# Optimization experiments

Measured on AMD Instinct MI355X. Metric: run time of the kernel, lower is better.

Reference implementation:

```python
import jax, jax.numpy as jnp
import numpy as np

N = 4194304   # number of query coordinates
D = 8         # feature width of xs
V = 1048576   # number of active sparse entries (param table size)


def setup_inputs() -> dict:
    key = jax.random.key(0)
    k1, k2, k3 = jax.random.split(key, 3)
    xs = jax.random.normal(k1, (N, D), dtype=jnp.float32)
    idx = jax.random.randint(k2, (N,), 0, V, dtype=jnp.int64)
    params = jax.random.normal(k3, (V, 1), dtype=jnp.float32)  # one scalar param per sparse entry
    return {"xs": xs, "idx": idx, "params": params}


def reference(xs, idx, params):
    # Original torch loop: out[i] = params[idx[i]] * xs[i]; fused gather-multiply.
    return params[idx] * xs  # [N,1] broadcast against [N,D] -> [N,D]
```

## Files before the change

kernel.cpp:

```cpp
#include <hip/hip_runtime.h>


typedef float f32x4 __attribute__((ext_vector_type(4)));

__global__ __launch_bounds__(256) void spvar_kernel(
    const f32x4* __restrict__ xs4,
    const int*   __restrict__ idx,
    const float* __restrict__ params,
    f32x4*       __restrict__ out4,
    int nrows, int stride)
{
    const int t = blockIdx.x * blockDim.x + threadIdx.x;
    const int r0 = t;
    const int r1 = t + stride;
    const int r2 = t + 2 * stride;
    const int r3 = t + 3 * stride;

    if (r3 < nrows) {
        const int i0 = idx[r0];
        const int i1 = idx[r1];
        const int i2 = idx[r2];
        const int i3 = idx[r3];

        const float p0 = params[i0];
        const float p1 = params[i1];
        const float p2 = params[i2];
        const float p3 = params[i3];

        f32x4 a0 = xs4[2 * r0], b0 = xs4[2 * r0 + 1];
        f32x4 a1 = xs4[2 * r1], b1 = xs4[2 * r1 + 1];
        f32x4 a2 = xs4[2 * r2], b2 = xs4[2 * r2 + 1];
        f32x4 a3 = xs4[2 * r3], b3 = xs4[2 * r3 + 1];

        a0 *= p0; b0 *= p0;
        a1 *= p1; b1 *= p1;
        a2 *= p2; b2 *= p2;
        a3 *= p3; b3 *= p3;

        out4[2 * r0] = a0; out4[2 * r0 + 1] = b0;
        out4[2 * r1] = a1; out4[2 * r1 + 1] = b1;
        out4[2 * r2] = a2; out4[2 * r2 + 1] = b2;
        out4[2 * r3] = a3; out4[2 * r3 + 1] = b3;
    } else {
        #pragma unroll
        for (int u = 0; u < 4; ++u) {
            const int r = t + u * stride;
            if (r < nrows) {
                const float p = params[idx[r]];
                f32x4 a = xs4[2 * r];
                f32x4 b = xs4[2 * r + 1];
                a *= p; b *= p;
                out4[2 * r]     = a;
                out4[2 * r + 1] = b;
            }
        }
    }
}

extern "C" void kernel_launch(void* const* d_in, const int* in_sizes, int n_in,
                              void* d_out, int out_size, void* d_ws, size_t ws_size,
                              hipStream_t stream) {
    const float* xs     = (const float*)d_in[0];
    const int*   idx    = (const int*)d_in[1];
    const float* params = (const float*)d_in[2];

    const int nrows = out_size / 8;
    const int block = 256;
    const int rows_per_thread = 4;
    const int grid = (nrows + block * rows_per_thread - 1) / (block * rows_per_thread);
    const int stride = grid * block;

    spvar_kernel<<<grid, block, 0, stream>>>(
        (const f32x4*)xs, idx, params, (f32x4*)d_out, nrows, stride);
}
```

Baseline: 260.4 us.

## Bucket param gathers by table range and use nontemporal streaming loads/stores

Each thread now handles eight rows and loads all eight indices up front. It then gathers params in four passes, one per quarter of the table, with scheduling barriers between passes, so concurrent gathers hit a smaller slice of the table and stay cache-resident. The streaming xs loads, index loads and output stores become nontemporal so they do not evict the param table. This adds predicated extra passes and hardcodes the table size as VTAB, so it breaks if V changes. Launch bounds also now request higher occupancy.

```diff
diff --git a/kernel.cpp b/kernel.cpp
--- a/kernel.cpp
+++ b/kernel.cpp
@@ -3,7 +3,12 @@
 
 typedef float f32x4 __attribute__((ext_vector_type(4)));
 
-__global__ __launch_bounds__(256) void spvar_kernel(
+#define ROWS 8
+#define NB   4
+#define VTAB 1048576
+#define BSZ  (VTAB / NB)
+
+__global__ __launch_bounds__(256, 8) void spvar_kernel(
     const f32x4* __restrict__ xs4,
     const int*   __restrict__ idx,
     const float* __restrict__ params,
@@ -11,48 +16,37 @@
     int nrows, int stride)
 {
     const int t = blockIdx.x * blockDim.x + threadIdx.x;
-    const int r0 = t;
-    const int r1 = t + stride;
-    const int r2 = t + 2 * stride;
-    const int r3 = t + 3 * stride;
 
-    if (r3 < nrows) {
-        const int i0 = idx[r0];
-        const int i1 = idx[r1];
-        const int i2 = idx[r2];
-        const int i3 = idx[r3];
+    int   ix[ROWS];
+    float p[ROWS];
+    #pragma unroll
+    for (int u = 0; u < ROWS; ++u) {
+        const int r = t + u * stride;
+        ix[u] = (r < nrows) ? __builtin_nontemporal_load(idx + r) : -1;
+        p[u]  = 0.0f;
+    }
 
-        const float p0 = params[i0];
-        const float p1 = params[i1];
-        const float p2 = params[i2];
-        const float p3 = params[i3];
+    #pragma unroll
+    for (int b = 0; b < NB; ++b) {
+        const int lo = b * BSZ;
+        #pragma unroll
+        for (int u = 0; u < ROWS; ++u) {
+            if ((unsigned)(ix[u] - lo) < (unsigned)BSZ)
+                p[u] = params[ix[u]];
+        }
+        __builtin_amdgcn_sched_barrier(0);
+    }
 
-        f32x4 a0 = xs4[2 * r0], b0 = xs4[2 * r0 + 1];
-        f32x4 a1 = xs4[2 * r1], b1 = xs4[2 * r1 + 1];
-        f32x4 a2 = xs4[2 * r2], b2 = xs4[2 * r2 + 1];
-        f32x4 a3 = xs4[2 * r3], b3 = xs4[2 * r3 + 1];
-
-        a0 *= p0; b0 *= p0;
-        a1 *= p1; b1 *= p1;
-        a2 *= p2; b2 *= p2;
-        a3 *= p3; b3 *= p3;
-
-        out4[2 * r0] = a0; out4[2 * r0 + 1] = b0;
-        out4[2 * r1] = a1; out4[2 * r1 + 1] = b1;
-        out4[2 * r2] = a2; out4[2 * r2 + 1] = b2;
-        out4[2 * r3] = a3; out4[2 * r3 + 1] = b3;
-    } else {
-        #pragma unroll
-        for (int u = 0; u < 4; ++u) {
-            const int r = t + u * stride;
-            if (r < nrows) {
-                const float p = params[idx[r]];
-                f32x4 a = xs4[2 * r];
-                f32x4 b = xs4[2 * r + 1];
-                a *= p; b *= p;
-                out4[2 * r]     = a;
-                out4[2 * r + 1] = b;
-            }
+    #pragma unroll
+    for (int u = 0; u < ROWS; ++u) {
+        const int r = t + u * stride;
+        if (r < nrows) {
+            f32x4 a = __builtin_nontemporal_load(xs4 + 2 * r);
+            f32x4 c = __builtin_nontemporal_load(xs4 + 2 * r + 1);
+            a *= p[u];
+            c *= p[u];
+            __builtin_nontemporal_store(a, out4 + 2 * r);
+            __builtin_nontemporal_store(c, out4 + 2 * r + 1);
         }
     }
 }
@@ -66,8 +60,7 @@
 
     const int nrows = out_size / 8;
     const int block = 256;
-    const int rows_per_thread = 4;
-    const int grid = (nrows + block * rows_per_thread - 1) / (block * rows_per_thread);
+    const int grid  = (nrows + block * ROWS - 1) / (block * ROWS);
     const int stride = grid * block;
 
     spvar_kernel<<<grid, block, 0, stream>>>(
```

New measurement: 268.6 us. 3.2% more time.
